# Kernel tuning notes

Hardware: AMD Instinct MI355X
Metric: run time of the kernel (lower is better)

Reference implementation:

```python
import jax, jax.numpy as jnp
import numpy as np

N, D, H = 2048, 1024, 16
HD = D // H  # 64
SCALE = float(np.sqrt(HD))  # sqrt(features // heads) = 8.0


def setup_inputs() -> dict:
    key = jax.random.key(0)
    ks = jax.random.split(key, 9)
    s = 0.02
    return {
        "x": jax.random.normal(ks[0], (N, D), dtype=jnp.float32),
        "Wq": jax.random.normal(ks[1], (D, D), dtype=jnp.float32) * s,
        "bq": jnp.zeros((D,), dtype=jnp.float32),
        "Wk": jax.random.normal(ks[2], (D, D), dtype=jnp.float32) * s,
        "bk": jnp.zeros((D,), dtype=jnp.float32),
        "Wv": jax.random.normal(ks[3], (D, D), dtype=jnp.float32) * s,
        "bv": jnp.zeros((D,), dtype=jnp.float32),
        "Wo": jax.random.normal(ks[4], (D, D), dtype=jnp.float32) * s,
        "bo": jnpp if False else jnp.zeros((D,), dtype=jnp.float32),
    }


def reference(x, Wq, bq, Wk, bk, Wv, bv, Wo, bo):
    # projections: [n, d]
    q = x @ Wq + bq
    k = x @ Wk + bk
    v = x @ Wv + bv
    # split heads: n (h d) -> h n d
    def split(t):
        return t.reshape(N, H, HD).transpose(1, 0, 2)
    q, k, v = split(q), split(k), split(v)
    # attention scores [h, n, n]
    scores = jnp.einsum('hnd,hmd->hnm', q, k) / SCALE
    # causal mask (tril), fill with dtype min as in original
    dmin = jnp.finfo(scores.dtype).min
    mask = jnp.tril(jnp.ones((N, N), dtype=bool))
    scores = jnp.where(mask, scores, dmin)
    attn = jax.nn.softmax(scores, axis=-1)
    # weighted sum, merge heads: h n d -> n (h d)
    out = jnp.einsum('hnm,hmd->hnd', attn, v)
    out = out.transpose(1, 0, 2).reshape(N, D)
    return out @ Wo + bo
```

## Files before the change

### kernel.cpp

```cpp
#include <hip/hip_runtime.h>
#include <hip/hip_bf16.h>
#include <math.h>

#define SA_N 2048
#define SA_D 1024
#define SA_H 16
#define SA_HD 64

typedef __attribute__((ext_vector_type(8))) short bf16x8;
typedef __attribute__((ext_vector_type(4))) float f32x4;
typedef __attribute__((address_space(3))) void lds_t;
typedef __attribute__((address_space(1))) void gmem_t;

__global__ __launch_bounds__(256) void cvt_bf16_kernel(
    const float* __restrict__ in, __hip_bfloat16* __restrict__ out, int n4)
{
    int i = blockIdx.x * 256 + threadIdx.x;
    if (i < n4) {
        float4 v = reinterpret_cast<const float4*>(in)[i];
        union { __hip_bfloat16 hh[4]; short4 s4; } u;
        u.hh[0] = __float2bfloat16(v.x);
        u.hh[1] = __float2bfloat16(v.y);
        u.hh[2] = __float2bfloat16(v.z);
        u.hh[3] = __float2bfloat16(v.w);
        reinterpret_cast<short4*>(out)[i] = u.s4;
    }
}

__global__ __launch_bounds__(256) void cvtT4_kernel(
    const float* __restrict__ W0, const float* __restrict__ W1,
    const float* __restrict__ W2, const float* __restrict__ W3,
    __hip_bfloat16* __restrict__ WtAll)
{
    const int z = blockIdx.z;
    const float* W = (z == 0) ? W0 : (z == 1) ? W1 : (z == 2) ? W2 : W3;
    __hip_bfloat16* Wt = WtAll + (size_t)z * SA_D * SA_D;
    __shared__ float t[32][33];
    const int c0 = blockIdx.x * 32, r0 = blockIdx.y * 32;
    const int tx = threadIdx.x & 31, ty = threadIdx.x >> 5;
#pragma unroll
    for (int p = 0; p < 4; ++p)
        t[ty + p * 8][tx] = W[(size_t)(r0 + ty + p * 8) * SA_D + c0 + tx];
    __syncthreads();
#pragma unroll
    for (int p = 0; p < 4; ++p)
        Wt[(size_t)(c0 + ty + p * 8) * SA_D + r0 + tx] = __float2bfloat16(t[tx][ty + p * 8]);
}

__device__ __forceinline__ void gemm_tile_body(
    const __hip_bfloat16* __restrict__ A,
    const __hip_bfloat16* __restrict__ Bt,
    const float* __restrict__ bias,
    void* __restrict__ Cout, int mode, int M, int Kdim, int Nout,
    char* As, char* Bs)
{
    const int tid = threadIdx.x;
    const int wave = tid >> 6, lane = tid & 63;
    const int m = lane & 15, quad = lane >> 4;
    const int wm = wave >> 1, wn = wave & 1;
    const int row0 = blockIdx.y * 64, col0 = blockIdx.x * 64;

    f32x4 acc[2][2];
#pragma unroll
    for (int i = 0; i < 2; ++i)
#pragma unroll
        for (int j = 0; j < 2; ++j) acc[i][j] = (f32x4){0.f, 0.f, 0.f, 0.f};

    const int sr = tid >> 3;
    const int sc = tid & 7;

    for (int k0 = 0; k0 < Kdim; k0 += 64) {
#pragma unroll
        for (int p = 0; p < 2; ++p) {
            const int r = p * 32 + sr;
            const int pc = (sc ^ (r & 7)) * 16;
            const char* ga = (const char*)(A + (size_t)(row0 + r) * Kdim + k0) + pc;
            __builtin_amdgcn_global_load_lds((gmem_t*)ga,
                (lds_t*)(As + p * 4096 + wave * 1024), 16, 0, 0);
            const char* gb = (const char*)(Bt + (size_t)(col0 + r) * Kdim + k0) + pc;
            __builtin_amdgcn_global_load_lds((gmem_t*)gb,
                (lds_t*)(Bs + p * 4096 + wave * 1024), 16, 0, 0);
        }
        __syncthreads();

#pragma unroll
        for (int s = 0; s < 2; ++s) {
            bf16x8 af[2], bfr[2];
#pragma unroll
            for (int mi = 0; mi < 2; ++mi) {
                const int row = wm * 32 + mi * 16 + m;
                const int pc = (s * 4 + quad) ^ (row & 7);
                af[mi] = *reinterpret_cast<const bf16x8*>(As + row * 128 + pc * 16);
            }
#pragma unroll
            for (int ni = 0; ni < 2; ++ni) {
                const int col = wn * 32 + ni * 16 + m;
                const int pc = (s * 4 + quad) ^ (col & 7);
                bfr[ni] = *reinterpret_cast<const bf16x8*>(Bs + col * 128 + pc * 16);
            }
#pragma unroll
            for (int mi = 0; mi < 2; ++mi)
#pragma unroll
                for (int ni = 0; ni < 2; ++ni)
                    acc[mi][ni] = __builtin_amdgcn_mfma_f32_16x16x32_bf16(
                        af[mi], bfr[ni], acc[mi][ni], 0, 0, 0);
        }
        __syncthreads();
    }

#pragma unroll
    for (int ni = 0; ni < 2; ++ni) {
        const int col = col0 + wn * 32 + ni * 16 + m;
        const float bv = bias[col];
#pragma unroll
        for (int mi = 0; mi < 2; ++mi) {
            const int rbase = row0 + wm * 32 + mi * 16 + quad * 4;
            if (mode == 0) {
#pragma unroll
                for (int reg = 0; reg < 4; ++reg)
                    ((float*)Cout)[(size_t)(rbase + reg) * Nout + col] =
                        acc[mi][ni][reg] + bv;
            } else if (mode == 1) {
#pragma unroll
                for (int reg = 0; reg < 4; ++reg)
                    ((__hip_bfloat16*)Cout)[(size_t)(rbase + reg) * Nout + col] =
                        __float2bfloat16(acc[mi][ni][reg] + bv);
            } else {
                union { __hip_bfloat16 hh[4]; short4 s4; } u;
#pragma unroll
                for (int reg = 0; reg < 4; ++reg)
                    u.hh[reg] = __float2bfloat16(acc[mi][ni][reg] + bv);
                *reinterpret_cast<short4*>(
                    &((__hip_bfloat16*)Cout)[(size_t)col * M + rbase]) = u.s4;
            }
        }
    }
}

__global__ __launch_bounds__(256) void gemm_qkv_kernel(
    const __hip_bfloat16* __restrict__ xbf, const __hip_bfloat16* __restrict__ WtAll,
    const float* __restrict__ bq, const float* __restrict__ bk, const float* __restrict__ bv,
    __hip_bfloat16* __restrict__ Qb, __hip_bfloat16* __restrict__ Kb,
    __hip_bfloat16* __restrict__ VtT)
{
    __shared__ __align__(16) char As[64 * 64 * 2];
    __shared__ __align__(16) char Bs[64 * 64 * 2];
    const int z = blockIdx.z;
    const __hip_bfloat16* Bt = WtAll + (size_t)z * SA_D * SA_D;
    const float* bias = (z == 0) ? bq : (z == 1) ? bk : bv;
    void* out = (z == 0) ? (void*)Qb : (z == 1) ? (void*)Kb : (void*)VtT;
    gemm_tile_body(xbf, Bt, bias, out, (z == 2) ? 2 : 1, SA_N, SA_D, SA_D, As, Bs);
}

__global__ __launch_bounds__(256) void gemm_out_kernel(
    const __hip_bfloat16* __restrict__ Abf, const __hip_bfloat16* __restrict__ Wt,
    const float* __restrict__ bo, float* __restrict__ out)
{
    __shared__ __align__(16) char As[64 * 64 * 2];
    __shared__ __align__(16) char Bs[64 * 64 * 2];
    gemm_tile_body(Abf, Wt, bo, out, 0, SA_N, SA_D, SA_D, As, Bs);
}

__global__ __launch_bounds__(256) void flash_mfma_kernel(
    const __hip_bfloat16* __restrict__ Qb,
    const __hip_bfloat16* __restrict__ Kb,
    const __hip_bfloat16* __restrict__ Vt,
    __hip_bfloat16* __restrict__ O)
{
    const int b = blockIdx.x;
    const int h = b & 15;
    const int qraw = b >> 4;
    const int qt = (qraw < 16) ? qraw : 47 - qraw;
    const int row0 = qt * 64;
    const int ntiles = (qt >> 1) + 1;

    const int tid = threadIdx.x;
    const int wave = tid >> 6, lane = tid & 63;
    const int ln = lane & 15, quad = lane >> 4;

    __shared__ __align__(16) char Qs[64 * 128];
    __shared__ __align__(16) char Ks[128 * 128];
    __shared__ __align__(16) char Vs[64 * 256];
    __shared__ __align__(16) char Ps[64 * 272];

#pragma unroll
    for (int p = 0; p < 2; ++p) {
        const int r = p * 32 + (tid >> 3);
        const int pc = ((tid & 7) ^ (r & 7)) * 16;
        const char* gq = (const char*)(Qb + (size_t)(row0 + r) * SA_D + h * SA_HD) + pc;
        __builtin_amdgcn_global_load_lds((gmem_t*)gq,
            (lds_t*)(Qs + p * 4096 + wave * 1024), 16, 0, 0);
    }

    f32x4 oacc[4], lacc;
#pragma unroll
    for (int g = 0; g < 4; ++g) oacc[g] = (f32x4){0.f, 0.f, 0.f, 0.f};
    lacc = (f32x4){0.f, 0.f, 0.f, 0.f};

    const float sc2 = 0.18033688011112042f;
    const short one_bf = (short)0x3F80;
    const bf16x8 ones = {one_bf, one_bf, one_bf, one_bf, one_bf, one_bf, one_bf, one_bf};

    for (int ktp = 0; ktp < ntiles; ++ktp) {
#pragma unroll
        for (int p = 0; p < 4; ++p) {
            const int r = p * 32 + (tid >> 3);
            const int pc = ((tid & 7) ^ (r & 7)) * 16;
            const char* gk = (const char*)(Kb + (size_t)(ktp * 128 + r) * SA_D + h * SA_HD) + pc;
            __builtin_amdgcn_global_load_lds((gmem_t*)gk,
                (lds_t*)(Ks + p * 4096 + wave * 1024), 16, 0, 0);
        }
#pragma unroll
        for (int p = 0; p < 4; ++p) {
            const int r = p * 16 + (tid >> 4);
            const int pc = ((tid & 15) ^ (r & 15)) * 16;
            const char* gv = (const char*)(Vt + (size_t)(h * SA_HD + r) * SA_N + ktp * 128) + pc;
            __builtin_amdgcn_global_load_lds((gmem_t*)gv,
                (lds_t*)(Vs + p * 4096 + wave * 1024), 16, 0, 0);
        }
        __syncthreads();

        f32x4 sacc[8];
#pragma unroll
        for (int g = 0; g < 8; ++g) sacc[g] = (f32x4){0.f, 0.f, 0.f, 0.f};
        const int mrow = wave * 16 + ln;
#pragma unroll
        for (int s = 0; s < 2; ++s) {
            const int pca = (s * 4 + quad) ^ (mrow & 7);
            bf16x8 af = *reinterpret_cast<const bf16x8*>(Qs + mrow * 128 + pca * 16);
#pragma unroll
            for (int g = 0; g < 8; ++g) {
                const int krow = g * 16 + ln;
                const int pcb = (s * 4 + quad) ^ (krow & 7);
                bf16x8 bf = *reinterpret_cast<const bf16x8*>(Ks + krow * 128 + pcb * 16);
                sacc[g] = __builtin_amdgcn_mfma_f32_16x16x32_bf16(af, bf, sacc[g], 0, 0, 0);
            }
        }

        const bool last = (ktp == ntiles - 1);
        const int prow_b = wave * 16 + quad * 4;
        const int qrow_b = row0 + prow_b;
#pragma unroll
        for (int g = 0; g < 8; ++g) {
            const int key = ktp * 128 + g * 16 + ln;
#pragma unroll
            for (int reg = 0; reg < 4; ++reg) {
                float p = exp2f(sacc[g][reg] * sc2);
                if (last && key > (qrow_b + reg)) p = 0.f;
                *reinterpret_cast<__hip_bfloat16*>(
                    Ps + (prow_b + reg) * 272 + (g * 16 + ln) * 2) = __float2bfloat16(p);
            }
        }

#pragma unroll
        for (int s2 = 0; s2 < 4; ++s2) {
            bf16x8 pf = *reinterpret_cast<const bf16x8*>(
                Ps + (wave * 16 + ln) * 272 + s2 * 64 + quad * 16);
            lacc = __builtin_amdgcn_mfma_f32_16x16x32_bf16(pf, ones, lacc, 0, 0, 0);
#pragma unroll
            for (int dg = 0; dg < 4; ++dg) {
                const int vrow = dg * 16 + ln;
                const int kc = s2 * 4 + quad;
                const int pcb = (kc ^ (vrow & 15)) * 16;
                bf16x8 vf = *reinterpret_cast<const bf16x8*>(Vs + vrow * 256 + pcb);
                oacc[dg] = __builtin_amdgcn_mfma_f32_16x16x32_bf16(pf, vf, oacc[dg], 0, 0, 0);
            }
        }
        __syncthreads();
    }

#pragma unroll
    for (int reg = 0; reg < 4; ++reg) {
        const int qrow = row0 + wave * 16 + quad * 4 + reg;
        const float inv = 1.0f / lacc[reg];
#pragma unroll
        for (int dg = 0; dg < 4; ++dg)
            O[(size_t)qrow * SA_D + h * SA_HD + dg * 16 + ln] =
                __float2bfloat16(oacc[dg][reg] * inv);
    }
}

extern "C" void kernel_launch(void* const* d_in, const int* in_sizes, int n_in,
                              void* d_out, int out_size, void* d_ws, size_t ws_size,
                              hipStream_t stream) {
    const float* x  = (const float*)d_in[0];
    const float* Wq = (const float*)d_in[1];
    const float* bq = (const float*)d_in[2];
    const float* Wk = (const float*)d_in[3];
    const float* bk = (const float*)d_in[4];
    const float* Wv = (const float*)d_in[5];
    const float* bv = (const float*)d_in[6];
    const float* Wo = (const float*)d_in[7];
    const float* bo = (const float*)d_in[8];
    float* out = (float*)d_out;

    const size_t ND = (size_t)SA_N * SA_D;
    const size_t DD = (size_t)SA_D * SA_D;
    __hip_bfloat16* xbf   = (__hip_bfloat16*)d_ws;
    __hip_bfloat16* WtAll = xbf + ND;
    __hip_bfloat16* Qb    = WtAll + 4 * DD;
    __hip_bfloat16* Kb    = Qb + ND;
    __hip_bfloat16* VtT   = Kb + ND;
    __hip_bfloat16* Abf   = VtT + ND;

    cvt_bf16_kernel<<<dim3((unsigned)(ND / 4 / 256)), 256, 0, stream>>>(x, xbf, (int)(ND / 4));
    cvtT4_kernel<<<dim3(SA_D / 32, SA_D / 32, 4), 256, 0, stream>>>(Wq, Wk, Wv, Wo, WtAll);
    gemm_qkv_kernel<<<dim3(SA_D / 64, SA_N / 64, 3), 256, 0, stream>>>(
        xbf, WtAll, bq, bk, bv, Qb, Kb, VtT);
    flash_mfma_kernel<<<dim3(512), 256, 0, stream>>>(Qb, Kb, VtT, Abf);
    gemm_out_kernel<<<dim3(SA_D / 64, SA_N / 64), 256, 0, stream>>>(
        Abf, WtAll + 3 * DD, bo, out);
}
```

Before: 154.0 us.

## Double-buffer K/V tiles in flash attention and enlarge GEMM tiles to 128x64

The attention kernel moves from 128-key tiles loaded synchronously to 64-key tiles in a two-slot K/V ring. The next tile is prefetched with global_load_lds while the current one is computed, and one barrier per iteration replaces two. Both projection GEMMs move from 64x64 to 128x64 output tiles, so each wave computes a 64x32 block and B tiles are reused across more rows. The larger GEMM tile halves the grid and raises register use, and the smaller attention tile adds more loop iterations and more masking work on the diagonal tile.

```diff
diff --git a/kernel.cpp b/kernel.cpp
--- a/kernel.cpp
+++ b/kernel.cpp
@@ -47,7 +47,7 @@
         Wt[(size_t)(c0 + ty + p * 8) * SA_D + r0 + tx] = __float2bfloat16(t[tx][ty + p * 8]);
 }
 
-__device__ __forceinline__ void gemm_tile_body(
+__device__ __forceinline__ void gemm_body_128x64(
     const __hip_bfloat16* __restrict__ A,
     const __hip_bfloat16* __restrict__ Bt,
     const float* __restrict__ bias,
@@ -58,11 +58,11 @@
     const int wave = tid >> 6, lane = tid & 63;
     const int m = lane & 15, quad = lane >> 4;
     const int wm = wave >> 1, wn = wave & 1;
-    const int row0 = blockIdx.y * 64, col0 = blockIdx.x * 64;
-
-    f32x4 acc[2][2];
-#pragma unroll
-    for (int i = 0; i < 2; ++i)
+    const int row0 = blockIdx.y * 128, col0 = blockIdx.x * 64;
+
+    f32x4 acc[4][2];
+#pragma unroll
+    for (int i = 0; i < 4; ++i)
 #pragma unroll
         for (int j = 0; j < 2; ++j) acc[i][j] = (f32x4){0.f, 0.f, 0.f, 0.f};
 
@@ -71,12 +71,17 @@
 
     for (int k0 = 0; k0 < Kdim; k0 += 64) {
 #pragma unroll
-        for (int p = 0; p < 2; ++p) {
+        for (int p = 0; p < 4; ++p) {
             const int r = p * 32 + sr;
             const int pc = (sc ^ (r & 7)) * 16;
             const char* ga = (const char*)(A + (size_t)(row0 + r) * Kdim + k0) + pc;
             __builtin_amdgcn_global_load_lds((gmem_t*)ga,
                 (lds_t*)(As + p * 4096 + wave * 1024), 16, 0, 0);
+        }
+#pragma unroll
+        for (int p = 0; p < 2; ++p) {
+            const int r = p * 32 + sr;
+            const int pc = (sc ^ (r & 7)) * 16;
             const char* gb = (const char*)(Bt + (size_t)(col0 + r) * Kdim + k0) + pc;
             __builtin_amdgcn_global_load_lds((gmem_t*)gb,
                 (lds_t*)(Bs + p * 4096 + wave * 1024), 16, 0, 0);
@@ -85,10 +90,10 @@
 
 #pragma unroll
         for (int s = 0; s < 2; ++s) {
-            bf16x8 af[2], bfr[2];
-#pragma unroll
-            for (int mi = 0; mi < 2; ++mi) {
-                const int row = wm * 32 + mi * 16 + m;
+            bf16x8 af[4], bfr[2];
+#pragma unroll
+            for (int mi = 0; mi < 4; ++mi) {
+                const int row = wm * 64 + mi * 16 + m;
                 const int pc = (s * 4 + quad) ^ (row & 7);
                 af[mi] = *reinterpret_cast<const bf16x8*>(As + row * 128 + pc * 16);
             }
@@ -99,7 +104,7 @@
                 bfr[ni] = *reinterpret_cast<const bf16x8*>(Bs + col * 128 + pc * 16);
             }
 #pragma unroll
-            for (int mi = 0; mi < 2; ++mi)
+            for (int mi = 0; mi < 4; ++mi)
 #pragma unroll
                 for (int ni = 0; ni < 2; ++ni)
                     acc[mi][ni] = __builtin_amdgcn_mfma_f32_16x16x32_bf16(
@@ -113,8 +118,8 @@
         const int col = col0 + wn * 32 + ni * 16 + m;
         const float bv = bias[col];
 #pragma unroll
-        for (int mi = 0; mi < 2; ++mi) {
-            const int rbase = row0 + wm * 32 + mi * 16 + quad * 4;
+        for (int mi = 0; mi < 4; ++mi) {
+            const int rbase = row0 + wm * 64 + mi * 16 + quad * 4;
             if (mode == 0) {
 #pragma unroll
                 for (int reg = 0; reg < 4; ++reg)
@@ -143,22 +148,22 @@
     __hip_bfloat16* __restrict__ Qb, __hip_bfloat16* __restrict__ Kb,
     __hip_bfloat16* __restrict__ VtT)
 {
-    __shared__ __align__(16) char As[64 * 64 * 2];
-    __shared__ __align__(16) char Bs[64 * 64 * 2];
+    __shared__ __align__(16) char As[128 * 128];
+    __shared__ __align__(16) char Bs[64 * 128];
     const int z = blockIdx.z;
     const __hip_bfloat16* Bt = WtAll + (size_t)z * SA_D * SA_D;
     const float* bias = (z == 0) ? bq : (z == 1) ? bk : bv;
     void* out = (z == 0) ? (void*)Qb : (z == 1) ? (void*)Kb : (void*)VtT;
-    gemm_tile_body(xbf, Bt, bias, out, (z == 2) ? 2 : 1, SA_N, SA_D, SA_D, As, Bs);
+    gemm_body_128x64(xbf, Bt, bias, out, (z == 2) ? 2 : 1, SA_N, SA_D, SA_D, As, Bs);
 }
 
 __global__ __launch_bounds__(256) void gemm_out_kernel(
     const __hip_bfloat16* __restrict__ Abf, const __hip_bfloat16* __restrict__ Wt,
     const float* __restrict__ bo, float* __restrict__ out)
 {
-    __shared__ __align__(16) char As[64 * 64 * 2];
-    __shared__ __align__(16) char Bs[64 * 64 * 2];
-    gemm_tile_body(Abf, Wt, bo, out, 0, SA_N, SA_D, SA_D, As, Bs);
+    __shared__ __align__(16) char As[128 * 128];
+    __shared__ __align__(16) char Bs[64 * 128];
+    gemm_body_128x64(Abf, Wt, bo, out, 0, SA_N, SA_D, SA_D, As, Bs);
 }
 
 __global__ __launch_bounds__(256) void flash_mfma_kernel(
@@ -172,26 +177,43 @@
     const int qraw = b >> 4;
     const int qt = (qraw < 16) ? qraw : 47 - qraw;
     const int row0 = qt * 64;
-    const int ntiles = (qt >> 1) + 1;
 
     const int tid = threadIdx.x;
     const int wave = tid >> 6, lane = tid & 63;
     const int ln = lane & 15, quad = lane >> 4;
 
     __shared__ __align__(16) char Qs[64 * 128];
-    __shared__ __align__(16) char Ks[128 * 128];
-    __shared__ __align__(16) char Vs[64 * 256];
-    __shared__ __align__(16) char Ps[64 * 272];
+    __shared__ __align__(16) char Ks[2][64 * 128];
+    __shared__ __align__(16) char Vs[2][64 * 128];
+    __shared__ __align__(16) char Ps[64 * 144];
+
+    const int sr = tid >> 3;
+    const int sc = tid & 7;
 
 #pragma unroll
     for (int p = 0; p < 2; ++p) {
-        const int r = p * 32 + (tid >> 3);
-        const int pc = ((tid & 7) ^ (r & 7)) * 16;
+        const int r = p * 32 + sr;
+        const int pc = (sc ^ (r & 7)) * 16;
         const char* gq = (const char*)(Qb + (size_t)(row0 + r) * SA_D + h * SA_HD) + pc;
         __builtin_amdgcn_global_load_lds((gmem_t*)gq,
             (lds_t*)(Qs + p * 4096 + wave * 1024), 16, 0, 0);
     }
 
+    auto stage = [&](int kt, int bb) {
+#pragma unroll
+        for (int p = 0; p < 2; ++p) {
+            const int r = p * 32 + sr;
+            const int pc = (sc ^ (r & 7)) * 16;
+            const char* gk = (const char*)(Kb + (size_t)(kt * 64 + r) * SA_D + h * SA_HD) + pc;
+            __builtin_amdgcn_global_load_lds((gmem_t*)gk,
+                (lds_t*)(Ks[bb] + p * 4096 + wave * 1024), 16, 0, 0);
+            const char* gv = (const char*)(Vt + (size_t)(h * SA_HD + r) * SA_N + kt * 64) + pc;
+            __builtin_amdgcn_global_load_lds((gmem_t*)gv,
+                (lds_t*)(Vs[bb] + p * 4096 + wave * 1024), 16, 0, 0);
+        }
+    };
+    stage(0, 0);
+
     f32x4 oacc[4], lacc;
 #pragma unroll
     for (int g = 0; g < 4; ++g) oacc[g] = (f32x4){0.f, 0.f, 0.f, 0.f};
@@ -201,72 +223,57 @@
     const short one_bf = (short)0x3F80;
     const bf16x8 ones = {one_bf, one_bf, one_bf, one_bf, one_bf, one_bf, one_bf, one_bf};
 
-    for (int ktp = 0; ktp < ntiles; ++ktp) {
-#pragma unroll
-        for (int p = 0; p < 4; ++p) {
-            const int r = p * 32 + (tid >> 3);
-            const int pc = ((tid & 7) ^ (r & 7)) * 16;
-            const char* gk = (const char*)(Kb + (size_t)(ktp * 128 + r) * SA_D + h * SA_HD) + pc;
-            __builtin_amdgcn_global_load_lds((gmem_t*)gk,
-                (lds_t*)(Ks + p * 4096 + wave * 1024), 16, 0, 0);
-        }
-#pragma unroll
-        for (int p = 0; p < 4; ++p) {
-            const int r = p * 16 + (tid >> 4);
-            const int pc = ((tid & 15) ^ (r & 15)) * 16;
-            const char* gv = (const char*)(Vt + (size_t)(h * SA_HD + r) * SA_N + ktp * 128) + pc;
-            __builtin_amdgcn_global_load_lds((gmem_t*)gv,
-                (lds_t*)(Vs + p * 4096 + wave * 1024), 16, 0, 0);
-        }
+    for (int kt = 0; kt <= qt; ++kt) {
         __syncthreads();
-
-        f32x4 sacc[8];
-#pragma unroll
-        for (int g = 0; g < 8; ++g) sacc[g] = (f32x4){0.f, 0.f, 0.f, 0.f};
+        if (kt < qt) stage(kt + 1, (kt + 1) & 1);
+        const char* K_ = Ks[kt & 1];
+        const char* V_ = Vs[kt & 1];
+
+        f32x4 sacc[4];
+#pragma unroll
+        for (int g = 0; g < 4; ++g) sacc[g] = (f32x4){0.f, 0.f, 0.f, 0.f};
         const int mrow = wave * 16 + ln;
 #pragma unroll
         for (int s = 0; s < 2; ++s) {
             const int pca = (s * 4 + quad) ^ (mrow & 7);
             bf16x8 af = *reinterpret_cast<const bf16x8*>(Qs + mrow * 128 + pca * 16);
 #pragma unroll
-            for (int g = 0; g < 8; ++g) {
+            for (int g = 0; g < 4; ++g) {
                 const int krow = g * 16 + ln;
                 const int pcb = (s * 4 + quad) ^ (krow & 7);
-                bf16x8 bf = *reinterpret_cast<const bf16x8*>(Ks + krow * 128 + pcb * 16);
+                bf16x8 bf = *reinterpret_cast<const bf16x8*>(K_ + krow * 128 + pcb * 16);
                 sacc[g] = __builtin_amdgcn_mfma_f32_16x16x32_bf16(af, bf, sacc[g], 0, 0, 0);
             }
         }
 
-        const bool last = (ktp == ntiles - 1);
+        const bool last = (kt == qt);
         const int prow_b = wave * 16 + quad * 4;
         const int qrow_b = row0 + prow_b;
 #pragma unroll
-        for (int g = 0; g < 8; ++g) {
-            const int key = ktp * 128 + g * 16 + ln;
+        for (int g = 0; g < 4; ++g) {
+            const int key = kt * 64 + g * 16 + ln;
 #pragma unroll
             for (int reg = 0; reg < 4; ++reg) {
                 float p = exp2f(sacc[g][reg] * sc2);
                 if (last && key > (qrow_b + reg)) p = 0.f;
                 *reinterpret_cast<__hip_bfloat16*>(
-                    Ps + (prow_b + reg) * 272 + (g * 16 + ln) * 2) = __float2bfloat16(p);
-            }
-        }
-
-#pragma unroll
-        for (int s2 = 0; s2 < 4; ++s2) {
+                    Ps + (prow_b + reg) * 144 + (g * 16 + ln) * 2) = __float2bfloat16(p);
+            }
+        }
+
+#pragma unroll
+        for (int s2 = 0; s2 < 2; ++s2) {
             bf16x8 pf = *reinterpret_cast<const bf16x8*>(
-                Ps + (wave * 16 + ln) * 272 + s2 * 64 + quad * 16);
+                Ps + (wave * 16 + ln) * 144 + s2 * 64 + quad * 16);
             lacc = __builtin_amdgcn_mfma_f32_16x16x32_bf16(pf, ones, lacc, 0, 0, 0);
 #pragma unroll
             for (int dg = 0; dg < 4; ++dg) {
                 const int vrow = dg * 16 + ln;
-                const int kc = s2 * 4 + quad;
-                const int pcb = (kc ^ (vrow & 15)) * 16;
-                bf16x8 vf = *reinterpret_cast<const bf16x8*>(Vs + vrow * 256 + pcb);
+                const int pcb = ((s2 * 4 + quad) ^ (vrow & 7)) * 16;
+                bf16x8 vf = *reinterpret_cast<const bf16x8*>(V_ + vrow * 128 + pcb);
                 oacc[dg] = __builtin_amdgcn_mfma_f32_16x16x32_bf16(pf, vf, oacc[dg], 0, 0, 0);
             }
         }
-        __syncthreads();
     }
 
 #pragma unroll
@@ -305,9 +312,9 @@
 
     cvt_bf16_kernel<<<dim3((unsigned)(ND / 4 / 256)), 256, 0, stream>>>(x, xbf, (int)(ND / 4));
     cvtT4_kernel<<<dim3(SA_D / 32, SA_D / 32, 4), 256, 0, stream>>>(Wq, Wk, Wv, Wo, WtAll);
-    gemm_qkv_kernel<<<dim3(SA_D / 64, SA_N / 64, 3), 256, 0, stream>>>(
+    gemm_qkv_kernel<<<dim3(SA_D / 64, SA_N / 128, 3), 256, 0, stream>>>(
         xbf, WtAll, bq, bk, bv, Qb, Kb, VtT);
     flash_mfma_kernel<<<dim3(512), 256, 0, stream>>>(Qb, Kb, VtT, Abf);
-    gemm_out_kernel<<<dim3(SA_D / 64, SA_N / 64), 256, 0, stream>>>(
+    gemm_out_kernel<<<dim3(SA_D / 64, SA_N / 128), 256, 0, stream>>>(
         Abf, WtAll + 3 * DD, bo, out);
 }
```

After: 163.1 us. +5.9%, slower.
